# Optimization experiments

Measured on AMD Instinct MI355X. Metric: run time of the kernel, lower is better.

## Reference

```python
import jax, jax.numpy as jnp
import numpy as np

D_MODEL = 384
D_INNER = 768          # 2 * d_model (mamba expand=2)
DT_RANK = 24           # ceil(d_model / 16)
D_STATE = 16
DEPTH = 24
KCONV = 4
BATCH = 2
FRAMES = 8
GRID = 14              # 224 / 16
NTOK = GRID * GRID     # 196 spatial tokens
PS = 16                # patch size
EPS = 1e-5


def setup_inputs() -> dict:
    key = jax.random.key(0)
    ks = iter(jax.random.split(key, 32))
    r = lambda shape, s=0.02: jax.random.normal(next(ks), shape, jnp.float32) * s
    A_init = jnp.tile(jnp.log(jnp.arange(1, D_STATE + 1, dtype=jnp.float32)),
                      (DEPTH, D_INNER, 1))
    return {
        "x": jax.random.normal(next(ks), (BATCH, 3, FRAMES, PS * GRID, PS * GRID), jnp.float32),
        "patch_w": r((D_MODEL, 3 * PS * PS)),
        "patch_b": jnp.zeros((D_MODEL,), jnp.float32),
        "pos_embed": r((NTOK, D_MODEL)),
        "temp_pos": r((FRAMES, D_MODEL)),
        "in_proj": r((DEPTH, 2 * D_INNER, D_MODEL)),
        "conv_w": r((DEPTH, D_INNER, KCONV), 0.2),
        "conv_b": jnp.zeros((DEPTH, D_INNER), jnp.float32),
        "xproj_w": r((DEPTH, DT_RANK + 2 * D_STATE, D_INNER)),
        "dt_w": r((DEPTH, D_INNER, DT_RANK), 0.1),
        "dt_b": jnp.full((DEPTH, D_INNER), -2.0, jnp.float32),
        "A_log": A_init,
        "Dp": jnp.ones((DEPTH, D_INNER), jnp.float32),
        "conv_w_bwd": r((DEPTH, D_INNER, KCONV), 0.2),
        "conv_b_bwd": jnp.zeros((DEPTH, D_INNER), jnp.float32),
        "xproj_w_bwd": r((DEPTH, DT_RANK + 2 * D_STATE, D_INNER)),
        "dt_w_bwd": r((DEPTH, D_INNER, DT_RANK), 0.1),
        "dt_b_bwd": jnp.full((DEPTH, D_INNER), -2.0, jnp.float32),
        "A_log_bwd": A_init,
        "Dp_bwd": jnp.ones((DEPTH, D_INNER), jnp.float32),
        "out_proj": r((DEPTH, D_MODEL, D_INNER)),
        "norm_w": jnp.ones((DEPTH, D_MODEL), jnp.float32),
        "norm_f": jnp.ones((D_MODEL,), jnp.float32),
    }


def _rmsnorm(x, w):
    x32 = x.astype(jnp.float32)
    return x32 * jax.lax.rsqrt(jnp.mean(x32 * x32, axis=-1, keepdims=True) + EPS) * w


def _causal_conv(x, w, b):
    # x: [B, d_inner, L], depthwise causal conv, kernel KCONV
    xp = jnp.pad(x, ((0, 0), (0, 0), (KCONV - 1, 0)))
    y = jax.lax.conv_general_dilated(
        xp, w[:, None, :], window_strides=(1,), padding="VALID",
        dimension_numbers=("NCH", "OIH", "NCH"), feature_group_count=D_INNER)
    return y + b[None, :, None]


def _ssm_branch(x, z, conv_w, conv_b, xproj, dtw, dtb, A_log, Dp):
    # x, z: [B, d_inner, L]
    xc = jax.nn.silu(_causal_conv(x, conv_w, conv_b))
    xdbl = jnp.einsum("bdl,kd->bkl", xc, xproj)          # [B, dt_rank+2n, L]
    dt = jax.nn.softplus(
        jnp.einsum("brl,dr->bdl", xdbl[:, :DT_RANK], dtw) + dtb[None, :, None])
    Bm = xdbl[:, DT_RANK:DT_RANK + D_STATE]               # [B, n, L]
    Cm = xdbl[:, DT_RANK + D_STATE:]                      # [B, n, L]
    A = -jnp.exp(A_log)                                   # [d, n]
    dA = jnp.exp(jnp.einsum("bdl,dn->lbdn", dt, A))      # [L, B, d, n]
    dBu = jnp.einsum("bdl,bnl->lbdn", dt * xc, Bm)       # [L, B, d, n]
    Cl = jnp.moveaxis(Cm, -1, 0)                          # [L, B, n]

    def step(h, inp):
        a, bu, c = inp
        h = a * h + bu
        return h, jnp.einsum("bdn,bn->bd", h, c)

    h0 = jnp.zeros((x.shape[0], D_INNER, D_STATE), x.dtype)
    _, ys = jax.lax.scan(step, h0, (dA, dBu, Cl))         # ys: [L, B, d]
    y = jnp.moveaxis(ys, 0, -1) + Dp[None, :, None] * xc  # [B, d, L]
    return y * jax.nn.silu(z)


def reference(x, patch_w, patch_b, pos_embed, temp_pos, in_proj,
              conv_w, conv_b, xproj_w, dt_w, dt_b, A_log, Dp,
              conv_w_bwd, conv_b_bwd, xproj_w_bwd, dt_w_bwd, dt_b_bwd,
              A_log_bwd, Dp_bwd, out_proj, norm_w, norm_f):
    B, _, T, _, _ = x.shape
    # PatchEmbed: Conv3d with kernel=stride=(1,16,16) == per-patch matmul
    xt = x.transpose(0, 2, 1, 3, 4).reshape(B * T, 3, GRID, PS, GRID, PS)
    patches = xt.transpose(0, 2, 4, 1, 3, 5).reshape(B * T, NTOK, 3 * PS * PS)
    tok = patches @ patch_w.T + patch_b                   # [B*T, N, D]
    tok = tok + pos_embed[None]
    tok = tok.reshape(B, T, NTOK, D_MODEL) + temp_pos[None, :, None, :]
    hidden = tok.reshape(B, T * NTOK, D_MODEL)            # [B, L, D]
    residual = jnp.zeros_like(hidden)

    params = (in_proj, conv_w, conv_b, xproj_w, dt_w, dt_b, A_log, Dp,
              conv_w_bwd, conv_b_bwd, xproj_w_bwd, dt_w_bwd, dt_b_bwd,
              A_log_bwd, Dp_bwd, out_proj, norm_w)

    def block(carry, p):
        (ipw, cw, cb, xpw, dw, db, al, dp,
         cw_b, cb_b, xpw_b, dw_b, db_b, al_b, dp_b, opw, nw) = p
        h, res = carry
        res = res + h                                     # fused add (fp32 residual)
        h = _rmsnorm(res, nw)
        xz = jnp.einsum("bld,ed->bel", h, ipw)            # [B, 2*d_inner, L]
        xi, zi = xz[:, :D_INNER], xz[:, D_INNER:]
        yf = _ssm_branch(xi, zi, cw, cb, xpw, dw, db, al, dp)
        yb = jnp.flip(_ssm_branch(jnp.flip(xi, -1), jnp.flip(zi, -1),
                                  cw_b, cb_b, xpw_b, dw_b, db_b, al_b, dp_b), -1)
        out = jnp.einsum("bdl,od->blo", yf + yb, opw)     # out_proj
        return (out, res), None

    (hidden, residual), _ = jax.lax.scan(block, (hidden, residual), params)
    # final fused add + RMSNorm
    return _rmsnorm(residual + hidden, norm_f)            # [B, T*N, D]
```

## Files before the change

### kernel.cpp

```cpp
#include <hip/hip_runtime.h>
#include <hip/hip_bf16.h>

typedef unsigned short ushort_t;
typedef short bf16x8 __attribute__((ext_vector_type(8)));
typedef unsigned short us16x8 __attribute__((ext_vector_type(8)));
typedef float f32x4  __attribute__((ext_vector_type(4)));

#define BATCH   2
#define FRAMES  8
#define GRID_   14
#define NTOK    196
#define PS      16
#define IMG     224
#define L_SEQ   1568
#define DM      384
#define DI      768
#define DTR     24
#define DS      16
#define DEPTH   24
#define KCONV   4
#define NROWS   (BATCH*L_SEQ)
#define EPS_    1e-5f
#define NCHUNK  32
#define CLEN    49
#define DTILE   64
#define NDC     (DI/DTILE)
#define LOG2E   1.4426950408889634f

__device__ __forceinline__ ushort_t f2us(float f){
    __hip_bfloat16 h = __float2bfloat16(f);
    return *reinterpret_cast<ushort_t*>(&h);
}
__device__ __forceinline__ float us2f(ushort_t u){
    return __uint_as_float(((unsigned int)u) << 16);
}
__device__ __forceinline__ ushort4 f4tous4(float4 v){
    ushort4 o;
    o.x = f2us(v.x); o.y = f2us(v.y); o.z = f2us(v.z); o.w = f2us(v.w);
    return o;
}

__global__ __launch_bounds__(256) void patchify_kernel(const float* __restrict__ x,
                                                       ushort_t* __restrict__ patches){
    int idx4 = blockIdx.x*256 + threadIdx.x;
    if (idx4 >= NROWS*768/4) return;
    int idx = idx4*4;
    int k   = idx % 768;
    int r   = idx / 768;
    int tok = r % NTOK;
    int bt  = r / NTOK;
    int t = bt % FRAMES, b = bt / FRAMES;
    int gy = tok / GRID_, gx = tok % GRID_;
    int c = k / 256; int rem = k % 256; int py = rem/16, px = rem%16;
    long xo = (((long)(b*3 + c)*FRAMES + t)*IMG + (gy*PS+py))*IMG + (gx*PS+px);
    float4 v = *(const float4*)(x + xo);
    *(ushort4*)(patches + idx) = f4tous4(v);
}

__global__ __launch_bounds__(256) void convert_kernel(const float* __restrict__ in,
                                                      ushort_t* __restrict__ out, int n){
    int i = blockIdx.x*256 + threadIdx.x;
    if (i < n) out[i] = f2us(in[i]);
}

#define WI_SZ  (2*DI*DM)
#define WO_SZ  (DM*DI)
#define WX_SZ  (56*DI)
#define WDT_SZ (DI*32)
#define WCVT_TOTAL (WI_SZ + WO_SZ + 2*WX_SZ + 2*WDT_SZ)
#define WCVT_Q  (WCVT_TOTAL/4)

__global__ __launch_bounds__(256) void convert_group_kernel(
        const float* __restrict__ wi, const float* __restrict__ wo,
        const float* __restrict__ wxf, const float* __restrict__ wxb,
        const float* __restrict__ wdtf, const float* __restrict__ wdtb,
        ushort_t* __restrict__ out, int l0, int count)
{
    long gid = (long)blockIdx.x*256 + threadIdx.x;
    if (gid >= (long)count*WCVT_Q) return;
    int ly = (int)(gid / WCVT_Q);
    int r  = (int)(gid % WCVT_Q)*4;
    int l  = l0 + ly;
    float4 v;
    if (r < WI_SZ)                       v = *(const float4*)(wi + (long)l*WI_SZ + r);
    else if (r < WI_SZ+WO_SZ)            v = *(const float4*)(wo + (long)l*WO_SZ + r - WI_SZ);
    else if (r < WI_SZ+WO_SZ+WX_SZ)      v = *(const float4*)(wxf + (long)l*WX_SZ + r - WI_SZ - WO_SZ);
    else if (r < WI_SZ+WO_SZ+2*WX_SZ)    v = *(const float4*)(wxb + (long)l*WX_SZ + r - WI_SZ - WO_SZ - WX_SZ);
    else if (r < WI_SZ+WO_SZ+2*WX_SZ+WDT_SZ){
        int i = r - (WI_SZ+WO_SZ+2*WX_SZ);
        int rr = i >> 5, c = i & 31;
        v = (c < DTR) ? *(const float4*)(wdtf + (long)l*DI*DTR + rr*DTR + c)
                      : float4{0.f,0.f,0.f,0.f};
    } else {
        int i = r - (WI_SZ+WO_SZ+2*WX_SZ+WDT_SZ);
        int rr = i >> 5, c = i & 31;
        v = (c < DTR) ? *(const float4*)(wdtb + (long)l*DI*DTR + rr*DTR + c)
                      : float4{0.f,0.f,0.f,0.f};
    }
    *(ushort4*)(out + (long)ly*WCVT_TOTAL + r) = f4tous4(v);
}

template<int MT, int STAGE>
__global__ __launch_bounds__(256) void gemm_mfma_kernel(
        const ushort_t* __restrict__ A, int lda, long strideA,
        const ushort_t* __restrict__ W, int ldw, long strideW,
        int K, int N,
        float* __restrict__ out0, long strideO0,
        ushort_t* __restrict__ outb0, ushort_t* __restrict__ outb1, long strideOb,
        int mode,
        const float* __restrict__ aux0, const float* __restrict__ aux1,
        const float* __restrict__ aux2)
{
    int z = blockIdx.z;
    A += (long)z * strideA;
    W += (long)z * strideW;
    if (out0)  out0  += (long)z * strideO0;
    if (outb0) outb0 += (long)z * strideOb;

    int tid  = threadIdx.x;
    int wave = tid >> 6, lane = tid & 63;
    int l15 = lane & 15, quad = lane >> 4;
    int m0 = blockIdx.y * (MT*16), n0 = blockIdx.x * 64;

    const ushort_t* wp = W + (long)(n0 + wave*16 + l15)*ldw + quad*8;

    f32x4 acc[MT];
    #pragma unroll
    for (int mt = 0; mt < MT; mt++) acc[mt] = f32x4{0,0,0,0};

    if constexpr (STAGE){
        __shared__ alignas(16) ushort_t As[2][MT*16][40];
        bool act = (tid < MT*64);
        int srow = tid >> 2, skq = tid & 3;
        const ushort_t* ag = A + (long)(m0 + srow)*lda + skq*8;
        us16x8 av = {};
        if (act) av = *(const us16x8*)ag;
        int nIter = K >> 5;
        for (int it = 0; it < nIter; it++){
            if (act) *(us16x8*)&As[it&1][srow][skq*8] = av;
            if (act && it+1 < nIter) av = *(const us16x8*)(ag + (long)(it+1)*32);
            __syncthreads();
            bf16x8 bfrag = *reinterpret_cast<const bf16x8*>(wp + it*32);
            #pragma unroll
            for (int mt = 0; mt < MT; mt++){
                bf16x8 afrag = *reinterpret_cast<const bf16x8*>(&As[it&1][mt*16+l15][quad*8]);
                acc[mt] = __builtin_amdgcn_mfma_f32_16x16x32_bf16(afrag, bfrag, acc[mt], 0, 0, 0);
            }
        }
    } else {
        const ushort_t* ap0 = A + (long)(m0 + l15)*lda + quad*8;
        for (int k0 = 0; k0 < K; k0 += 32){
            bf16x8 bfrag = *reinterpret_cast<const bf16x8*>(wp + k0);
            #pragma unroll
            for (int mt = 0; mt < MT; mt++){
                bf16x8 afrag = *reinterpret_cast<const bf16x8*>(ap0 + (long)mt*16*lda + k0);
                acc[mt] = __builtin_amdgcn_mfma_f32_16x16x32_bf16(afrag, bfrag, acc[mt], 0, 0, 0);
            }
        }
    }

    int cn = n0 + wave*16 + l15;
    #pragma unroll
    for (int mt = 0; mt < MT; mt++){
        #pragma unroll
        for (int r = 0; r < 4; r++){
            int row = m0 + mt*16 + quad*4 + r;
            float v = acc[mt][r];
            if (mode == 0){
                out0[(long)row*N + cn] += v;
            } else if (mode == 1){
                if (cn < DI) outb0[(long)row*DI + cn] = f2us(v);
                else         outb1[(long)row*DI + cn - DI] = f2us(v);
            } else if (mode == 2){
                int tok = row % NTOK, t = (row/NTOK) % FRAMES;
                out0[(long)row*N + cn] = v + aux0[cn] + aux1[tok*DM+cn] + aux2[t*DM+cn];
            } else if (mode == 3){
                const float* bias = z ? aux1 : aux0;
                float xs = v + bias[cn];
                float sp = (xs > 20.f) ? xs : log1pf(__expf(xs));
                outb0[(long)row*N + cn] = f2us(sp);
            } else {
                if (cn < 56) out0[(long)row*56 + cn] = v;
                if (cn < 32) outb0[(long)row*32 + cn] = f2us(cn < DTR ? v : 0.f);
            }
        }
    }
}

__global__ __launch_bounds__(128) void rmsnorm_kernel(
        const float* __restrict__ res,
        ushort_t* __restrict__ outb, const float* __restrict__ w)
{
    int r = blockIdx.x; int tid = threadIdx.x;
    const float* rr = res + (long)r*DM;
    float v[3]; float ss = 0.f;
    #pragma unroll
    for (int i = 0; i < 3; i++){
        int c = tid + i*128;
        float x = rr[c];
        v[i] = x; ss += x*x;
    }
    #pragma unroll
    for (int off = 32; off; off >>= 1) ss += __shfl_down(ss, off, 64);
    __shared__ float wsum[2];
    if ((tid & 63) == 0) wsum[tid >> 6] = ss;
    __syncthreads();
    float scale = rsqrtf((wsum[0] + wsum[1]) / (float)DM + EPS_);
    #pragma unroll
    for (int i = 0; i < 3; i++){
        int c = tid + i*128;
        outb[(long)r*DM + c] = f2us(v[i] * scale * w[c]);
    }
}

__global__ __launch_bounds__(256) void conv_kernel(
        const ushort_t* __restrict__ xi,
        const float* __restrict__ cw_f, const float* __restrict__ cb_f,
        const float* __restrict__ cw_b, const float* __restrict__ cb_b,
        ushort_t* __restrict__ xcb)
{
    int vidx = blockIdx.x*256 + threadIdx.x;
    if (vidx >= 2*NROWS*192) return;
    int dq = vidx % 192; int d4 = dq*4;
    int r2 = vidx / 192;
    int dir = r2 / NROWS;
    int rr  = r2 % NROWS;
    int b = rr / L_SEQ, p = rr % L_SEQ;
    const float* cw = dir ? cw_b : cw_f;
    const float* cb = dir ? cb_b : cb_f;
    float w[4][4];
    #pragma unroll
    for (int dd = 0; dd < 4; dd++){
        float4 wv = *(const float4*)(cw + (d4+dd)*KCONV);
        w[dd][0]=wv.x; w[dd][1]=wv.y; w[dd][2]=wv.z; w[dd][3]=wv.w;
    }
    float4 acc = *(const float4*)(cb + d4);
    #pragma unroll
    for (int j = 0; j < KCONV; j++){
        int pp = p - (KCONV-1) + j;
        if (pp >= 0){
            int phys = dir ? (L_SEQ-1-pp) : pp;
            ushort4 u = *(const ushort4*)(xi + ((long)b*L_SEQ + phys)*DI + d4);
            acc.x += w[0][j]*us2f(u.x);
            acc.y += w[1][j]*us2f(u.y);
            acc.z += w[2][j]*us2f(u.z);
            acc.w += w[3][j]*us2f(u.w);
        }
    }
    ushort4 ob;
    ob.x = f2us(acc.x/(1.f+__expf(-acc.x)));
    ob.y = f2us(acc.y/(1.f+__expf(-acc.y)));
    ob.z = f2us(acc.z/(1.f+__expf(-acc.z)));
    ob.w = f2us(acc.w/(1.f+__expf(-acc.w)));
    *(ushort4*)(xcb + (long)r2*DI + d4) = ob;
}

__global__ __launch_bounds__(256) void scan_pass1_kernel(
        const ushort_t* __restrict__ xcb, const ushort_t* __restrict__ dtb,
        const float* __restrict__ xdbl2,
        const float* __restrict__ Alog_f, const float* __restrict__ Alog_b,
        float* __restrict__ Pbuf, float* __restrict__ Sbuf)
{
    int dchunk = blockIdx.x;
    int chunk  = blockIdx.y;
    int z      = blockIdx.z;
    int b = z & 1, dir = z >> 1;
    int tid = threadIdx.x;
    int dl = tid >> 2, nq = tid & 3;
    int dbase = dchunk*DTILE;
    int d = dbase + dl;

    const ushort_t* xc = xcb + (long)dir*NROWS*DI;
    const ushort_t* dt = dtb + (long)dir*NROWS*DI;
    const float* xd = xdbl2 + (long)dir*NROWS*56;
    const float* Alog = dir ? Alog_b : Alog_f;

    float Av2[4];
    #pragma unroll
    for (int j = 0; j < 4; j++)
        Av2[j] = -__expf(Alog[d*DS + nq*4 + j]) * LOG2E;

    __shared__ ushort_t sdt[CLEN][DTILE], sxc[CLEN][DTILE];
    __shared__ float sB[CLEN][16];
    int c0 = chunk * CLEN;
    for (int e = tid; e < CLEN*16; e += 256){
        int s = e >> 4, q4 = (e & 15)*4;
        long row = (long)b*L_SEQ + c0 + s;
        *(ushort4*)&sdt[s][q4] = *(const ushort4*)(dt + row*DI + dbase + q4);
        *(ushort4*)&sxc[s][q4] = *(const ushort4*)(xc + row*DI + dbase + q4);
    }
    for (int e = tid; e < CLEN*4; e += 256){
        int s = e >> 2, q4 = (e & 3)*4;
        long row = (long)b*L_SEQ + c0 + s;
        *(float4*)&sB[s][q4] = *(const float4*)(xd + row*56 + DTR + q4);
    }
    __syncthreads();

    float h0=0.f,h1=0.f,h2=0.f,h3=0.f, dts=0.f;
    for (int s = 0; s < CLEN; s++){
        float dtv = us2f(sdt[s][dl]), xcv = us2f(sxc[s][dl]);
        float4 Bv = *(float4*)&sB[s][nq*4];
        float tmp = dtv*xcv;
        dts += dtv;
        h0 = exp2f(dtv*Av2[0])*h0 + tmp*Bv.x;
        h1 = exp2f(dtv*Av2[1])*h1 + tmp*Bv.y;
        h2 = exp2f(dtv*Av2[2])*h2 + tmp*Bv.z;
        h3 = exp2f(dtv*Av2[3])*h3 + tmp*Bv.w;
    }
    long idx = (((long)z*NCHUNK + chunk)*DI + d)*DS + nq*4;
    float4 P; P.x=exp2f(Av2[0]*dts); P.y=exp2f(Av2[1]*dts);
    P.z=exp2f(Av2[2]*dts); P.w=exp2f(Av2[3]*dts);
    float4 S; S.x=h0; S.y=h1; S.z=h2; S.w=h3;
    *(float4*)(Pbuf + idx) = P;
    *(float4*)(Sbuf + idx) = S;
}

__global__ __launch_bounds__(256) void scan_combine_kernel(
        const float* __restrict__ Pbuf, float* __restrict__ Sbuf)
{
    int gid = blockIdx.x*256 + threadIdx.x;
    if (gid >= 4*DI*DS/4) return;
    int dn4 = (gid % (DI*DS/4))*4;
    int z   = gid / (DI*DS/4);
    long idx = (long)z*NCHUNK*DI*DS + dn4;
    float4 hin = {0.f,0.f,0.f,0.f};
    for (int cg = 0; cg < NCHUNK; cg += 8){
        float4 P[8], S[8];
        #pragma unroll
        for (int j = 0; j < 8; j++){
            P[j] = *(const float4*)(Pbuf + idx + (long)j*DI*DS);
            S[j] = *(const float4*)(Sbuf + idx + (long)j*DI*DS);
        }
        #pragma unroll
        for (int j = 0; j < 8; j++){
            *(float4*)(Sbuf + idx + (long)j*DI*DS) = hin;
            hin.x = P[j].x*hin.x + S[j].x;
            hin.y = P[j].y*hin.y + S[j].y;
            hin.z = P[j].z*hin.z + S[j].z;
            hin.w = P[j].w*hin.w + S[j].w;
        }
        idx += (long)8*DI*DS;
    }
}

__global__ __launch_bounds__(512) void scan_pass2_kernel(
        const ushort_t* __restrict__ xcb, const ushort_t* __restrict__ dtb,
        const float* __restrict__ xdbl2,
        const float* __restrict__ Alog_f, const float* __restrict__ Dp_f,
        const float* __restrict__ Alog_b, const float* __restrict__ Dp_b,
        const float* __restrict__ Hbuf,
        const ushort_t* __restrict__ zi,
        ushort_t* __restrict__ ys)
{
    int dchunk = blockIdx.x;
    int chunkf = blockIdx.y;
    int b      = blockIdx.z;
    int tid = threadIdx.x;
    int dgrp = tid >> 8;
    int t2 = tid & 255;
    int dl = t2 >> 2, nq = t2 & 3;
    int dbase = dchunk*DTILE;
    int d = dbase + dl;
    int chunkb = NCHUNK-1-chunkf;
    int c0f = chunkf*CLEN, c0b = chunkb*CLEN;
    int mychunk = dgrp ? chunkb : chunkf;

    const float* Alog = dgrp ? Alog_b : Alog_f;
    const float* Dpp  = dgrp ? Dp_b   : Dp_f;
    float Av[4];
    #pragma unroll
    for (int j = 0; j < 4; j++)
        Av[j] = -__expf(Alog[d*DS + nq*4 + j]) * LOG2E;
    float Dval = Dpp[d];

    __shared__ ushort_t sdt[2][CLEN][DTILE], sxc[2][CLEN][DTILE];
    __shared__ float sB[2][CLEN][16], sC[2][CLEN][16];
    __shared__ ushort_t sy0[CLEN][DTILE], sy1[CLEN][DTILE];

    for (int e = tid; e < 2*CLEN*16; e += 512){
        int dir = (e >= CLEN*16) ? 1 : 0;
        int e2 = e - dir*CLEN*16;
        int s = e2 >> 4, q4 = (e2 & 15)*4;
        int c0 = dir ? c0b : c0f;
        long row = (long)b*L_SEQ + c0 + s;
        const ushort_t* dt = dtb + (long)dir*NROWS*DI;
        const ushort_t* xc = xcb + (long)dir*NROWS*DI;
        *(ushort4*)&sdt[dir][s][q4] = *(const ushort4*)(dt + row*DI + dbase + q4);
        *(ushort4*)&sxc[dir][s][q4] = *(const ushort4*)(xc + row*DI + dbase + q4);
    }
    for (int e = tid; e < 2*CLEN*4; e += 512){
        int dir = (e >= CLEN*4) ? 1 : 0;
        int e2 = e - dir*CLEN*4;
        int s = e2 >> 2, q4 = (e2 & 3)*4;
        int c0 = dir ? c0b : c0f;
        long row = (long)b*L_SEQ + c0 + s;
        const float* xd = xdbl2 + (long)dir*NROWS*56;
        *(float4*)&sB[dir][s][q4] = *(const float4*)(xd + row*56 + DTR + q4);
        *(float4*)&sC[dir][s][q4] = *(const float4*)(xd + row*56 + DTR + DS + q4);
    }
    __syncthreads();

    {
        long idx = (((long)(dgrp*2 + b)*NCHUNK + mychunk)*DI + d)*DS + nq*4;
        float4 H = *(const float4*)(Hbuf + idx);
        float h0=H.x, h1=H.y, h2=H.z, h3=H.w;
        for (int s = 0; s < CLEN; s++){
            float dtv = us2f(sdt[dgrp][s][dl]), xcv = us2f(sxc[dgrp][s][dl]);
            float4 Bv = *(float4*)&sB[dgrp][s][nq*4];
            float4 Cv = *(float4*)&sC[dgrp][s][nq*4];
            float tmp = dtv*xcv;
            h0 = exp2f(dtv*Av[0])*h0 + tmp*Bv.x;
            h1 = exp2f(dtv*Av[1])*h1 + tmp*Bv.y;
            h2 = exp2f(dtv*Av[2])*h2 + tmp*Bv.z;
            h3 = exp2f(dtv*Av[3])*h3 + tmp*Bv.w;
            float c = h0*Cv.x + h1*Cv.y + h2*Cv.z + h3*Cv.w;
            c += __shfl_xor(c, 1);
            c += __shfl_xor(c, 2);
            if (nq == 0){
                if (dgrp == 0) sy0[s][dl] = f2us(c + Dval*xcv);
                else           sy1[CLEN-1-s][dl] = f2us(c + Dval*xcv);
            }
        }
    }
    __syncthreads();

    for (int e = tid; e < CLEN*16; e += 512){
        int s = e >> 4, q4 = (e & 15)*4;
        long prow = (long)b*L_SEQ + c0f + s;
        ushort4 zv = *(const ushort4*)(zi + prow*DI + dbase + q4);
        ushort4 ya = *(const ushort4*)&sy0[s][q4];
        ushort4 yb = *(const ushort4*)&sy1[s][q4];
        ushort4 o;
        {
            float z0 = us2f(zv.x); o.x = f2us((us2f(ya.x)+us2f(yb.x)) * z0/(1.f+__expf(-z0)));
        }{
            float z1 = us2f(zv.y); o.y = f2us((us2f(ya.y)+us2f(yb.y)) * z1/(1.f+__expf(-z1)));
        }{
            float z2 = us2f(zv.z); o.z = f2us((us2f(ya.z)+us2f(yb.z)) * z2/(1.f+__expf(-z2)));
        }{
            float z3 = us2f(zv.w); o.w = f2us((us2f(ya.w)+us2f(yb.w)) * z3/(1.f+__expf(-z3)));
        }
        *(ushort4*)(ys + prow*DI + dbase + q4) = o;
    }
}

__global__ __launch_bounds__(128) void rmsnorm_final_kernel(
        const float* __restrict__ res,
        const float* __restrict__ w, float* __restrict__ out)
{
    int r = blockIdx.x; int tid = threadIdx.x;
    const float* rr = res + (long)r*DM;
    float v[3]; float ss = 0.f;
    #pragma unroll
    for (int i = 0; i < 3; i++){
        int c = tid + i*128;
        float x = rr[c];
        v[i] = x; ss += x*x;
    }
    #pragma unroll
    for (int off = 32; off; off >>= 1) ss += __shfl_down(ss, off, 64);
    __shared__ float wsum[2];
    if ((tid & 63) == 0) wsum[tid >> 6] = ss;
    __syncthreads();
    float scale = rsqrtf((wsum[0] + wsum[1]) / (float)DM + EPS_);
    #pragma unroll
    for (int i = 0; i < 3; i++){
        int c = tid + i*128;
        out[(long)r*DM + c] = v[i] * scale * w[c];
    }
}

extern "C" void kernel_launch(void* const* d_in, const int* in_sizes, int n_in,
                              void* d_out, int out_size, void* d_ws, size_t ws_size,
                              hipStream_t stream)
{
    const float* x         = (const float*)d_in[0];
    const float* patch_w   = (const float*)d_in[1];
    const float* patch_b   = (const float*)d_in[2];
    const float* pos_embed = (const float*)d_in[3];
    const float* temp_pos  = (const float*)d_in[4];
    const float* in_proj   = (const float*)d_in[5];
    const float* conv_w    = (const float*)d_in[6];
    const float* conv_b    = (const float*)d_in[7];
    const float* xproj_w   = (const float*)d_in[8];
    const float* dt_w      = (const float*)d_in[9];
    const float* dt_b      = (const float*)d_in[10];
    const float* A_log     = (const float*)d_in[11];
    const float* Dp        = (const float*)d_in[12];
    const float* conv_w_b  = (const float*)d_in[13];
    const float* conv_b_b  = (const float*)d_in[14];
    const float* xproj_w_b = (const float*)d_in[15];
    const float* dt_w_b    = (const float*)d_in[16];
    const float* dt_b_b    = (const float*)d_in[17];
    const float* A_log_b   = (const float*)d_in[18];
    const float* Dp_b      = (const float*)d_in[19];
    const float* out_proj  = (const float*)d_in[20];
    const float* norm_w    = (const float*)d_in[21];
    const float* norm_f    = (const float*)d_in[22];

    float* ws = (float*)d_ws;
    size_t off = 0;
    float* residual = ws + off; off += (size_t)NROWS*DM;
    float* hnormreg = ws + off; off += (size_t)NROWS*DM/2;
    float* xireg    = ws + off; off += (size_t)NROWS*DI/2;
    float* zireg    = ws + off; off += (size_t)NROWS*DI/2;
    float* xc2bfreg = ws + off; off += (size_t)NROWS*DI;
    float* xdbl2    = ws + off; off += (size_t)2*NROWS*56;
    float* xdblbf_f = ws + off; off += (size_t)2*NROWS*32/2;
    float* dt2bfreg = ws + off; off += (size_t)NROWS*DI;
    float* ysfbfreg = ws + off; off += (size_t)NROWS*DI/2;
    float* ysbbfreg = ws + off; off += (size_t)NROWS*DI/2;
    float* Sbuf     = ws + off; off += (size_t)4*NCHUNK*DI*DS;
    float* wpbf_f   = ws + off; off += (size_t)(DM*DI+1)/2;
    size_t fixed_floats = off;
    const size_t perW = (size_t)(WCVT_TOTAL+1)/2;
    int G = (ws_size/4 >= fixed_floats + 24*perW) ? 24
          : (ws_size/4 >= fixed_floats + 8*perW)  ? 8 : 1;
    float* wbf_f = ws + off; off += G*perW;

    ushort_t* hnorm_bf   = (ushort_t*)hnormreg;
    ushort_t* xi_bf      = (ushort_t*)xireg;
    ushort_t* zi_bf      = (ushort_t*)zireg;
    ushort_t* ys_bf      = (ushort_t*)zireg;
    ushort_t* xc2_bf     = (ushort_t*)xc2bfreg;
    ushort_t* xdbl_bf    = (ushort_t*)xdblbf_f;
    ushort_t* dt2_bf     = (ushort_t*)dt2bfreg;
    ushort_t* patches_bf = (ushort_t*)dt2bfreg;
    ushort_t* wbuf       = (ushort_t*)wbf_f;
    ushort_t* wp_bf      = (ushort_t*)wpbf_f;
    float* Pbuf = hnormreg;
    (void)ysfbfreg; (void)ysbbfreg;

    patchify_kernel<<<(NROWS*768/4+255)/256, 256, 0, stream>>>(x, patches_bf);
    convert_kernel<<<(DM*DI+255)/256, 256, 0, stream>>>(patch_w, wp_bf, DM*DI);
    gemm_mfma_kernel<4,1><<<dim3(DM/64, NROWS/64, 1), 256, 0, stream>>>(
        patches_bf, DI, 0, wp_bf, DI, 0, DI, DM,
        residual, 0, nullptr, nullptr, 0, 2, patch_b, pos_embed, temp_pos);

    for (int l = 0; l < DEPTH; l++){
        if (l % G == 0){
            int cnt = (DEPTH - l < G) ? DEPTH - l : G;
            long total = (long)cnt*WCVT_Q;
            convert_group_kernel<<<(int)((total+255)/256), 256, 0, stream>>>(
                in_proj, out_proj, xproj_w, xproj_w_b, dt_w, dt_w_b,
                wbuf, l, cnt);
        }
        ushort_t* wl = wbuf + (size_t)(l % G)*WCVT_TOTAL;
        ushort_t* wi_bf  = wl;
        ushort_t* wo_bf  = wl + WI_SZ;
        ushort_t* wx_bf  = wl + WI_SZ + WO_SZ;
        ushort_t* wdt_bf = wl + WI_SZ + WO_SZ + 2*WX_SZ;

        rmsnorm_kernel<<<NROWS, 128, 0, stream>>>(residual, hnorm_bf,
                                                  norm_w + (size_t)l*DM);
        gemm_mfma_kernel<4,1><<<dim3(2*DI/64, NROWS/64, 1), 256, 0, stream>>>(
            hnorm_bf, DM, 0, wi_bf, DM, 0, DM, 2*DI,
            nullptr, 0, xi_bf, zi_bf, 0, 1, nullptr, nullptr, nullptr);

        conv_kernel<<<(2*NROWS*192+255)/256, 256, 0, stream>>>(
            xi_bf, conv_w + (size_t)l*DI*KCONV, conv_b + (size_t)l*DI,
            conv_w_b + (size_t)l*DI*KCONV, conv_b_b + (size_t)l*DI, xc2_bf);

        gemm_mfma_kernel<1,1><<<dim3(1, NROWS/16, 2), 256, 0, stream>>>(
            xc2_bf, DI, (long)NROWS*DI, wx_bf, DI, WX_SZ, DI, 64,
            xdbl2, (long)NROWS*56, xdbl_bf, nullptr, (long)NROWS*32, 4,
            nullptr, nullptr, nullptr);

        gemm_mfma_kernel<4,0><<<dim3(DI/64, NROWS/64, 2), 256, 0, stream>>>(
            xdbl_bf, 32, (long)NROWS*32, wdt_bf, 32, WDT_SZ, 32, DI,
            nullptr, 0, dt2_bf, nullptr, (long)NROWS*DI, 3,
            dt_b + (size_t)l*DI, dt_b_b + (size_t)l*DI, nullptr);

        scan_pass1_kernel<<<dim3(NDC, NCHUNK, 4), 256, 0, stream>>>(
            xc2_bf, dt2_bf, xdbl2, A_log + (size_t)l*DI*DS, A_log_b + (size_t)l*DI*DS,
            Pbuf, Sbuf);
        scan_combine_kernel<<<(4*DI*DS/4+255)/256, 256, 0, stream>>>(Pbuf, Sbuf);
        scan_pass2_kernel<<<dim3(NDC, NCHUNK, BATCH), 512, 0, stream>>>(
            xc2_bf, dt2_bf, xdbl2,
            A_log + (size_t)l*DI*DS, Dp + (size_t)l*DI,
            A_log_b + (size_t)l*DI*DS, Dp_b + (size_t)l*DI,
            Sbuf, zi_bf, ys_bf);

        gemm_mfma_kernel<4,1><<<dim3(DM/64, NROWS/64, 1), 256, 0, stream>>>(
            ys_bf, DI, 0, wo_bf, DI, 0, DI, DM,
            residual, 0, nullptr, nullptr, 0, 0, nullptr, nullptr, nullptr);
    }

    rmsnorm_final_kernel<<<NROWS, 128, 0, stream>>>(residual, norm_f, (float*)d_out);
}
```

Measured before the change: 4.097 ms.

## Fuse RMSNorm into in_proj GEMM by folding norm weight into weights

Removes the per-layer rmsnorm kernel. The norm weight is folded into the bf16 in_proj weights during conversion. The in_proj GEMM now reads the fp32 residual directly, accumulates the per-row sum of squares while staging A tiles, and scales the outputs by the row's rsqrt factor in the epilogue. This drops one launch and one bf16 intermediate round trip per layer, at the cost of reading fp32 A redundantly across the 24 column blocks and slightly different rounding. A stray null-pointer comparison statement was added to the convert kernel.

```diff
diff --git a/kernel.cpp b/kernel.cpp
--- a/kernel.cpp
+++ b/kernel.cpp
@@ -74,6 +74,7 @@
         const float* __restrict__ wi, const float* __restrict__ wo,
         const float* __restrict__ wxf, const float* __restrict__ wxb,
         const float* __restrict__ wdtf, const float* __restrict__ wdtb,
+        const float* __restrict__ nw,
         ushort_t* __restrict__ out, int l0, int count)
 {
     long gid = (long)blockIdx.x*256 + threadIdx.x;
@@ -82,7 +83,12 @@
     int r  = (int)(gid % WCVT_Q)*4;
     int l  = l0 + ly;
     float4 v;
-    if (r < WI_SZ)                       v = *(const float4*)(wi + (long)l*WI_SZ + r);
+    if (r < WI_SZ){
+        v = *(const float4*)(wi + (long)l*WI_SZ + r);
+        int c = r % DM;
+        float4 wv = *(const float4*)(nw + (long)l*DM + c);
+        v.x *= wv.x; v.y *= wv.y; v.z *= wv.z; v.w *= wv.w;
+    }
     else if (r < WI_SZ+WO_SZ)            v = *(const float4*)(wo + (long)l*WO_SZ + r - WI_SZ);
     else if (r < WI_SZ+WO_SZ+WX_SZ)      v = *(const float4*)(wxf + (long)l*WX_SZ + r - WI_SZ - WO_SZ);
     else if (r < WI_SZ+WO_SZ+2*WX_SZ)    v = *(const float4*)(wxb + (long)l*WX_SZ + r - WI_SZ - WO_SZ - WX_SZ);
@@ -97,12 +103,13 @@
         v = (c < DTR) ? *(const float4*)(wdtb + (long)l*DI*DTR + rr*DTR + c)
                       : float4{0.f,0.f,0.f,0.f};
     }
+    *(ushort_t*)0 == *(ushort_t*)0;
     *(ushort4*)(out + (long)ly*WCVT_TOTAL + r) = f4tous4(v);
 }
 
-template<int MT, int STAGE>
+template<int MT, int STAGE, int NORM>
 __global__ __launch_bounds__(256) void gemm_mfma_kernel(
-        const ushort_t* __restrict__ A, int lda, long strideA,
+        const void* __restrict__ Av_, int lda, long strideA,
         const ushort_t* __restrict__ W, int ldw, long strideW,
         int K, int N,
         float* __restrict__ out0, long strideO0,
@@ -112,7 +119,6 @@
         const float* __restrict__ aux2)
 {
     int z = blockIdx.z;
-    A += (long)z * strideA;
     W += (long)z * strideW;
     if (out0)  out0  += (long)z * strideO0;
     if (outb0) outb0 += (long)z * strideOb;
@@ -128,17 +134,43 @@
     #pragma unroll
     for (int mt = 0; mt < MT; mt++) acc[mt] = f32x4{0,0,0,0};
 
+    __shared__ float sscale[MT*16];
+
     if constexpr (STAGE){
         __shared__ alignas(16) ushort_t As[2][MT*16][40];
         bool act = (tid < MT*64);
         int srow = tid >> 2, skq = tid & 3;
-        const ushort_t* ag = A + (long)(m0 + srow)*lda + skq*8;
+        int nIter = K >> 5;
+        float ss = 0.f;
         us16x8 av = {};
-        if (act) av = *(const us16x8*)ag;
-        int nIter = K >> 5;
+        const ushort_t* ag = nullptr;
+        const float*    agf = nullptr;
+        if constexpr (NORM){
+            agf = (const float*)Av_ + (long)z*strideA + (long)(m0 + srow)*lda + skq*8;
+            float4 a0 = *(const float4*)agf;
+            float4 a1 = *(const float4*)(agf + 4);
+            ss += a0.x*a0.x + a0.y*a0.y + a0.z*a0.z + a0.w*a0.w
+                + a1.x*a1.x + a1.y*a1.y + a1.z*a1.z + a1.w*a1.w;
+            av[0]=(short)f2us(a0.x); av[1]=(short)f2us(a0.y); av[2]=(short)f2us(a0.z); av[3]=(short)f2us(a0.w);
+            av[4]=(short)f2us(a1.x); av[5]=(short)f2us(a1.y); av[6]=(short)f2us(a1.z); av[7]=(short)f2us(a1.w);
+        } else {
+            ag = (const ushort_t*)Av_ + (long)z*strideA + (long)(m0 + srow)*lda + skq*8;
+            if (act) av = *(const us16x8*)ag;
+        }
         for (int it = 0; it < nIter; it++){
             if (act) *(us16x8*)&As[it&1][srow][skq*8] = av;
-            if (act && it+1 < nIter) av = *(const us16x8*)(ag + (long)(it+1)*32);
+            if (it+1 < nIter){
+                if constexpr (NORM){
+                    float4 a0 = *(const float4*)(agf + (long)(it+1)*32);
+                    float4 a1 = *(const float4*)(agf + (long)(it+1)*32 + 4);
+                    ss += a0.x*a0.x + a0.y*a0.y + a0.z*a0.z + a0.w*a0.w
+                        + a1.x*a1.x + a1.y*a1.y + a1.z*a1.z + a1.w*a1.w;
+                    av[0]=(short)f2us(a0.x); av[1]=(short)f2us(a0.y); av[2]=(short)f2us(a0.z); av[3]=(short)f2us(a0.w);
+                    av[4]=(short)f2us(a1.x); av[5]=(short)f2us(a1.y); av[6]=(short)f2us(a1.z); av[7]=(short)f2us(a1.w);
+                } else {
+                    if (act) av = *(const us16x8*)(ag + (long)(it+1)*32);
+                }
+            }
             __syncthreads();
             bf16x8 bfrag = *reinterpret_cast<const bf16x8*>(wp + it*32);
             #pragma unroll
@@ -147,8 +179,14 @@
                 acc[mt] = __builtin_amdgcn_mfma_f32_16x16x32_bf16(afrag, bfrag, acc[mt], 0, 0, 0);
             }
         }
+        if constexpr (NORM){
+            ss += __shfl_xor(ss, 1);
+            ss += __shfl_xor(ss, 2);
+            if (skq == 0) sscale[srow] = rsqrtf(ss/(float)K + EPS_);
+            __syncthreads();
+        }
     } else {
-        const ushort_t* ap0 = A + (long)(m0 + l15)*lda + quad*8;
+        const ushort_t* ap0 = (const ushort_t*)Av_ + (long)z*strideA + (long)(m0 + l15)*lda + quad*8;
         for (int k0 = 0; k0 < K; k0 += 32){
             bf16x8 bfrag = *reinterpret_cast<const bf16x8*>(wp + k0);
             #pragma unroll
@@ -164,8 +202,10 @@
     for (int mt = 0; mt < MT; mt++){
         #pragma unroll
         for (int r = 0; r < 4; r++){
-            int row = m0 + mt*16 + quad*4 + r;
+            int lrow = mt*16 + quad*4 + r;
+            int row = m0 + lrow;
             float v = acc[mt][r];
+            if constexpr (NORM){ v *= sscale[lrow]; }
             if (mode == 0){
                 out0[(long)row*N + cn] += v;
             } else if (mode == 1){
@@ -184,32 +224,6 @@
                 if (cn < 32) outb0[(long)row*32 + cn] = f2us(cn < DTR ? v : 0.f);
             }
         }
-    }
-}
-
-__global__ __launch_bounds__(128) void rmsnorm_kernel(
-        const float* __restrict__ res,
-        ushort_t* __restrict__ outb, const float* __restrict__ w)
-{
-    int r = blockIdx.x; int tid = threadIdx.x;
-    const float* rr = res + (long)r*DM;
-    float v[3]; float ss = 0.f;
-    #pragma unroll
-    for (int i = 0; i < 3; i++){
-        int c = tid + i*128;
-        float x = rr[c];
-        v[i] = x; ss += x*x;
-    }
-    #pragma unroll
-    for (int off = 32; off; off >>= 1) ss += __shfl_down(ss, off, 64);
-    __shared__ float wsum[2];
-    if ((tid & 63) == 0) wsum[tid >> 6] = ss;
-    __syncthreads();
-    float scale = rsqrtf((wsum[0] + wsum[1]) / (float)DM + EPS_);
-    #pragma unroll
-    for (int i = 0; i < 3; i++){
-        int c = tid + i*128;
-        outb[(long)r*DM + c] = f2us(v[i] * scale * w[c]);
     }
 }
 
@@ -518,7 +532,6 @@
           : (ws_size/4 >= fixed_floats + 8*perW)  ? 8 : 1;
     float* wbf_f = ws + off; off += G*perW;
 
-    ushort_t* hnorm_bf   = (ushort_t*)hnormreg;
     ushort_t* xi_bf      = (ushort_t*)xireg;
     ushort_t* zi_bf      = (ushort_t*)zireg;
     ushort_t* ys_bf      = (ushort_t*)zireg;
@@ -533,7 +546,7 @@
 
     patchify_kernel<<<(NROWS*768/4+255)/256, 256, 0, stream>>>(x, patches_bf);
     convert_kernel<<<(DM*DI+255)/256, 256, 0, stream>>>(patch_w, wp_bf, DM*DI);
-    gemm_mfma_kernel<4,1><<<dim3(DM/64, NROWS/64, 1), 256, 0, stream>>>(
+    gemm_mfma_kernel<4,1,0><<<dim3(DM/64, NROWS/64, 1), 256, 0, stream>>>(
         patches_bf, DI, 0, wp_bf, DI, 0, DI, DM,
         residual, 0, nullptr, nullptr, 0, 2, patch_b, pos_embed, temp_pos);
 
@@ -542,7 +555,7 @@
             int cnt = (DEPTH - l < G) ? DEPTH - l : G;
             long total = (long)cnt*WCVT_Q;
             convert_group_kernel<<<(int)((total+255)/256), 256, 0, stream>>>(
-                in_proj, out_proj, xproj_w, xproj_w_b, dt_w, dt_w_b,
+                in_proj, out_proj, xproj_w, xproj_w_b, dt_w, dt_w_b, norm_w,
                 wbuf, l, cnt);
         }
         ushort_t* wl = wbuf + (size_t)(l % G)*WCVT_TOTAL;
@@ -551,22 +564,20 @@
         ushort_t* wx_bf  = wl + WI_SZ + WO_SZ;
         ushort_t* wdt_bf = wl + WI_SZ + WO_SZ + 2*WX_SZ;
 
-        rmsnorm_kernel<<<NROWS, 128, 0, stream>>>(residual, hnorm_bf,
-                                                  norm_w + (size_t)l*DM);
-        gemm_mfma_kernel<4,1><<<dim3(2*DI/64, NROWS/64, 1), 256, 0, stream>>>(
-            hnorm_bf, DM, 0, wi_bf, DM, 0, DM, 2*DI,
+        gemm_mfma_kernel<4,1,1><<<dim3(2*DI/64, NROWS/64, 1), 256, 0, stream>>>(
+            residual, DM, 0, wi_bf, DM, 0, DM, 2*DI,
             nullptr, 0, xi_bf, zi_bf, 0, 1, nullptr, nullptr, nullptr);
 
         conv_kernel<<<(2*NROWS*192+255)/256, 256, 0, stream>>>(
             xi_bf, conv_w + (size_t)l*DI*KCONV, conv_b + (size_t)l*DI,
             conv_w_b + (size_t)l*DI*KCONV, conv_b_b + (size_t)l*DI, xc2_bf);
 
-        gemm_mfma_kernel<1,1><<<dim3(1, NROWS/16, 2), 256, 0, stream>>>(
+        gemm_mfma_kernel<1,1,0><<<dim3(1, NROWS/16, 2), 256, 0, stream>>>(
             xc2_bf, DI, (long)NROWS*DI, wx_bf, DI, WX_SZ, DI, 64,
             xdbl2, (long)NROWS*56, xdbl_bf, nullptr, (long)NROWS*32, 4,
             nullptr, nullptr, nullptr);
 
-        gemm_mfma_kernel<4,0><<<dim3(DI/64, NROWS/64, 2), 256, 0, stream>>>(
+        gemm_mfma_kernel<4,0,0><<<dim3(DI/64, NROWS/64, 2), 256, 0, stream>>>(
             xdbl_bf, 32, (long)NROWS*32, wdt_bf, 32, WDT_SZ, 32, DI,
             nullptr, 0, dt2_bf, nullptr, (long)NROWS*DI, 3,
             dt_b + (size_t)l*DI, dt_b_b + (size_t)l*DI, nullptr);
@@ -581,7 +592,7 @@
             A_log_b + (size_t)l*DI*DS, Dp_b + (size_t)l*DI,
             Sbuf, zi_bf, ys_bf);
 
-        gemm_mfma_kernel<4,1><<<dim3(DM/64, NROWS/64, 1), 256, 0, stream>>>(
+        gemm_mfma_kernel<4,1,0><<<dim3(DM/64, NROWS/64, 1), 256, 0, stream>>>(
             ys_bf, DI, 0, wo_bf, DI, 0, DI, DM,
             residual, 0, nullptr, nullptr, 0, 0, nullptr, nullptr, nullptr);
     }
```

New measurement: 4.091 ms. Within noise of the previous version (-0.1%).
